# Kernel optimization log

Measured on AMD Instinct MI355X. Metric: run time of the kernel, lower is better.

## Reference

```python
import jax, jax.numpy as jnp
import numpy as np

NU, NS, NG, NW, NT = 100000, 50000, 50, 20000, 10
C, F = 64, 384

def setup_inputs() -> dict:
    key = jax.random.key(0)
    ks = jax.random.split(key, 24)
    s = 0.02
    inp = {
        'reviews': jax.random.normal(ks[0], (NU, F), jnp.float32),
        'overview': jax.random.normal(ks[1], (NS, F), jnp.float32),
        'g_emb': jax.random.normal(ks[2], (NG, C), jnp.float32) * s,
        'w_emb': jax.random.normal(ks[3], (NW, C), jnp.float32) * s,
        't_emb': jax.random.normal(ks[4], (NT, C), jnp.float32) * s,
        'Wu': jax.random.normal(ks[5], (C, F), jnp.float32) * s,
        'bu': jnp.zeros((C,), jnp.float32),
        'Ws': jax.random.normal(ks[6], (C, F), jnp.float32) * s,
        'bs': jnp.zeros((C,), jnp.float32),
        'Wl1': jax.random.normal(ks[7], (8, C, C), jnp.float32) * s,
        'bl1': jnp.zeros((8, C), jnp.float32),
        'Wr1': jax.random.normal(ks[8], (8, C, C), jnp.float32) * s,
        'Wl2': jax.random.normal(ks[9], (8, C, C), jnp.float32) * s,
        'bl2': jnp.zeros((8, C), jnp.float32),
        'Wr2': jax.random.normal(ks[10], (8, C, C), jnp.float32) * s,
        'e_u2s': jnp.stack([jax.random.randint(ks[11], (1000000,), 0, NU, jnp.int32),
                             jax.random.randint(ks[12], (1000000,), 0, NS, jnp.int32)]),
        'e_g2s': jnp.stack([jax.random.randint(ks[13], (150000,), 0, NG, jnp.int32),
                             jax.random.randint(ks[14], (150000,), 0, NS, jnp.int32)]),
        'e_w2s': jnp.stack([jax.random.randint(ks[15], (50000,), 0, NW, jnp.int32),
                             jax.random.randint(ks[16], (50000,), 0, NS, jnp.int32)]),
        'e_t2s': jnp.stack([jax.random.randint(ks[17], (50000,), 0, NT, jnp.int32),
                             jax.random.randint(ks[18], (50000,), 0, NS, jnp.int32)]),
        'eli': jnp.stack([jax.random.randint(ks[19], (200000,), 0, NU, jnp.int32),
                           jax.random.randint(ks[20], (200000,), 0, NS, jnp.int32)]),
    }
    return inp


def _sage_conv(x_src, x_dst, src, dst, Wl, bl, Wr):
    # PyG SAGEConv: lin_l(mean_{neighbors} x_src) + lin_r(x_dst); lin_r has no bias
    n_dst = x_dst.shape[0]
    msg = x_src[src]                                   # [E, C] gather
    agg = jax.ops.segment_sum(msg, dst, num_segments=n_dst)
    cnt = jax.ops.segment_sum(jnp.ones((src.shape[0], 1), x_src.dtype), dst, num_segments=n_dst)
    mean = agg / jnp.maximum(cnt, 1.0)
    return mean @ Wl.T + bl + x_dst @ Wr.T


def _hetero_layer(x, ets, Wl, bl, Wr):
    # to_hetero: per-edge-type SAGEConv, sum-aggregate over edge types per dst node type
    out = {k: None for k in x}
    for i, (st, dt, src, dst) in enumerate(ets):
        o = _sage_conv(x[st], x[dt], src, dst, Wl[i], bl[i], Wr[i])
        out[dt] = o if out[dt] is None else out[dt] + o
    return out


def _forward(reviews, overview, g_emb, w_emb, t_emb, Wu, bu, Ws, bs,
             Wl1, bl1, Wr1, Wl2, bl2, Wr2, e_u2s, e_g2s, e_w2s, e_t2s, eli):
    x = {
        'users': reviews @ Wu.T + bu,
        'series': overview @ Ws.T + bs,
        'genres': g_emb,
        'writer': w_emb,
        'type': t_emb,
    }
    # edge types (fixed order matching the weight stacking): fwd + reverse (ToUndirected)
    ets = [
        ('users', 'series', e_u2s[0], e_u2s[1]),
        ('series', 'users', e_u2s[1], e_u2s[0]),
        ('genres', 'series', e_g2s[0], e_g2s[1]),
        ('series', 'genres', e_g2s[1], e_g2s[0]),
        ('writer', 'series', e_w2s[0], e_w2s[1]),
        ('series', 'writer', e_w2s[1], e_w2s[0]),
        ('type', 'series', e_t2s[0], e_t2s[1]),
        ('series', 'type', e_t2s[1], e_t2s[0]),
    ]
    x = _hetero_layer(x, ets, Wl1, bl1, Wr1)
    x = {k: jax.nn.relu(v) for k, v in x.items()}
    x = _hetero_layer(x, ets, Wl2, bl2, Wr2)
    # Classifier: dot-product scoring on edge_label_index
    src = x['users'][eli[0]]
    dst = x['series'][eli[1]]
    return (src * dst).sum(axis=-1)


def reference(reviews, overview, g_emb, w_emb, t_emb, Wu, bu, Ws, bs,
              Wl1, bl1, Wr1, Wl2, bl2, Wr2, e_u2s, e_g2s, e_w2s, e_t2s, eli):
    return _forward(reviews, overview, g_emb, w_emb, t_emb, Wu, bu, Ws, bs,
                    Wl1, bl1, Wr1, Wl2, bl2, Wr2, e_u2s, e_g2s, e_w2s, e_t2s, eli)
```

## Files before the change

kernel.cpp:

```cpp
#include <hip/hip_runtime.h>

#define NU 100000
#define NS 50000
#define NG 50
#define NW 20000
#define NT 10
#define CDIM 64
#define FDIM 384

typedef short bf16x8 __attribute__((ext_vector_type(8)));
typedef float f32x4 __attribute__((ext_vector_type(4)));
typedef unsigned short ushort;
typedef unsigned int uint;

#define CHUNK 128
#define CSHIFT 7
#define CMASK 127
#define NBINS 2503
#define PSTRIDE 800
#define BTOT 352
#define CTOT 2503
#define W_TOTAL 188416
#define WPB 736

struct PrepArgs {
  const int* src[6];
  const int* dst[6];
  int E[6];
  int nchunk[6];
  int nb[6];
  int cbase[7];
  int bbase[7];
  int cstart[7];
  int* partial;
  int* chunktot;
  int* choff;
  int* bucket[6];
  int* adj[6];
  int* off[6];
};

struct WArgs {
  const float* Wu; const float* Wsp;
  const float* Wl1; const float* Wr1;
  const float* Wl2; const float* Wr2;
  ushort* S;
};

__device__ __forceinline__ void hist_body(const PrepArgs& a, int b, int t, int* bins) {
  int ty = 0;
  while (b >= a.bbase[ty + 1]) ++ty;
  int bl = b - a.bbase[ty], B = a.bbase[ty + 1] - a.bbase[ty];
  int n = a.nchunk[ty], E = a.E[ty];
  const int* __restrict__ dst = a.dst[ty];
  for (int i = t; i < n; i += 256) bins[i] = 0;
  __syncthreads();
  for (int i = bl * 256 + t; i < E; i += B * 256) atomicAdd(&bins[dst[i] >> CSHIFT], 1);
  __syncthreads();
  int* row = a.partial + (size_t)b * PSTRIDE;
  for (int i = t; i < n; i += 256) row[i] = bins[i];
}

__device__ __forceinline__ void scanb_body(const PrepArgs& a, int bin) {
  if (bin >= NBINS) return;
  int ty = 0;
  while (bin >= a.cbase[ty + 1]) ++ty;
  int l = bin - a.cbase[ty];
  int run = 0;
  for (int b = a.bbase[ty]; b < a.bbase[ty + 1]; ++b) {
    int* p = a.partial + (size_t)b * PSTRIDE + l;
    int v = *p;
    *p = run;
    run += v;
  }
  a.chunktot[bin] = run;
}

__device__ __forceinline__ void scanc_body(const PrepArgs& a, int ty, int t, int* sc) {
  int n = a.nchunk[ty];
  int chunk = (n + 255) / 256;
  int lo = t * chunk, hi = min(n, lo + chunk);
  const int* __restrict__ cnt = a.chunktot + a.cbase[ty];
  int s = 0;
  for (int i = lo; i < hi; ++i) s += cnt[i];
  sc[t] = s;
  __syncthreads();
  for (int d = 1; d < 256; d <<= 1) {
    int u = (t >= d) ? sc[t - d] : 0;
    __syncthreads();
    sc[t] += u;
    __syncthreads();
  }
  int* choff = a.choff + a.cbase[ty] + ty;
  int carry = (t > 0) ? sc[t - 1] : 0;
  for (int i = lo; i < hi; ++i) { choff[i] = carry; carry += cnt[i]; }
  if (t == 255) choff[n] = sc[255];
}

__device__ __forceinline__ void fill_body(const PrepArgs& a, int b, int t, int* bins, int* base) {
  int ty = 0;
  while (b >= a.bbase[ty + 1]) ++ty;
  int bl = b - a.bbase[ty], B = a.bbase[ty + 1] - a.bbase[ty];
  int n = a.nchunk[ty], E = a.E[ty];
  const int* __restrict__ dst = a.dst[ty];
  const int* __restrict__ src = a.src[ty];
  int* __restrict__ bucket = a.bucket[ty];
  const int* choff = a.choff + a.cbase[ty] + ty;
  const int* prow = a.partial + (size_t)b * PSTRIDE;
  for (int i = t; i < n; i += 256) { bins[i] = 0; base[i] = choff[i] + prow[i]; }
  __syncthreads();
  for (int i = bl * 256 + t; i < E; i += B * 256) {
    int d = dst[i];
    int l = d >> CSHIFT;
    int r = atomicAdd(&bins[l], 1);
    bucket[base[l] + r] = (src[i] << CSHIFT) | (d & CMASK);
  }
}

__device__ __forceinline__ void csr_body(const PrepArgs& a, int b, int t,
                                         int* bins, int* sc, int* basea) {
  int ty = 0;
  while (b >= a.cstart[ty + 1]) ++ty;
  int c = b - a.cstart[ty];
  const int* __restrict__ bucket = a.bucket[ty];
  const int* choff = a.choff + a.cbase[ty] + ty;
  int beg = choff[c], end = choff[c + 1];
  if (t < CHUNK) bins[t] = 0;
  __syncthreads();
  for (int i = beg + t; i < end; i += 256) atomicAdd(&bins[bucket[i] & CMASK], 1);
  __syncthreads();
  int v = (t < CHUNK) ? bins[t] : 0;
  if (t < CHUNK) sc[t] = v;
  __syncthreads();
#pragma unroll
  for (int d = 1; d < CHUNK; d <<= 1) {
    int u = (t < CHUNK && t >= d) ? sc[t - d] : 0;
    __syncthreads();
    if (t < CHUNK) sc[t] += u;
    __syncthreads();
  }
  if (t < CHUNK) { basea[t] = beg + sc[t] - v; bins[t] = basea[t]; }
  __syncthreads();
  int gbase = c * CHUNK;
  int nb = a.nb[ty];
  if (t < CHUNK && gbase + t < nb) a.off[ty][gbase + t] = basea[t];
  if (b == a.cstart[ty + 1] - 1 && t == 0) a.off[ty][nb] = choff[a.nchunk[ty]];
  int* __restrict__ adj = a.adj[ty];
  for (int i = beg + t; i < end; i += 256) {
    int pk = bucket[i];
    int r = atomicAdd(&bins[pk & CMASK], 1);
    adj[r] = pk >> CSHIFT;
  }
}

__device__ __forceinline__ int swz_src(int u, int F) {
  int p = u >> 11;
  int nt = (u >> 9) & 3;
  int lane = (u >> 3) & 63;
  int j = u & 7;
  int row = nt * 16 + (lane & 15);
  int col = p * 32 + ((lane >> 4) << 3) + j;
  return row * F + col;
}

__device__ __forceinline__ void wprep_body(const WArgs& w, int i) {
  if (i >= W_TOTAL) return;
  float v;
  size_t hbase, lbase;
  int u;
  if (i < 24576) {
    u = i; hbase = 0; lbase = 24576;
    v = w.Wu[swz_src(u, FDIM)];
  } else if (i < 49152) {
    u = i - 24576; hbase = 49152; lbase = 73728;
    v = w.Wsp[swz_src(u, FDIM)];
  } else {
    int j = i - 49152;
    int layer = j / 69632;
    j %= 69632;
    const float* Wl = layer ? w.Wl2 : w.Wl1;
    const float* Wr = layer ? w.Wr2 : w.Wr1;
    size_t base = 98304 + (size_t)layer * 139264;
    if (j < 32768) {
      int s = j >> 12; u = j & 4095;
      hbase = base + (size_t)s * 4096; lbase = base + 32768 + (size_t)s * 4096;
      v = Wl[s * 4096 + swz_src(u, 64)];
    } else if (j < 65536) {
      int q = j - 32768; int s = q >> 12; u = q & 4095;
      hbase = base + 65536 + (size_t)s * 4096; lbase = base + 98304 + (size_t)s * 4096;
      v = Wr[s * 4096 + swz_src(u, 64)];
    } else {
      u = j - 65536;
      hbase = base + 131072; lbase = base + 135168;
      int si = swz_src(u, 64);
      v = Wr[si] + Wr[8192 + si] + Wr[16384 + si] + Wr[24576 + si];
    }
  }
  uint b = __float_as_uint(v);
  uint h = b & 0xFFFF0000u;
  float r = v - __uint_as_float(h);
  w.S[hbase + u] = (ushort)(h >> 16);
  w.S[lbase + u] = (ushort)(__float_as_uint(r) >> 16);
}

__device__ __forceinline__ void csr_gather_body(const int* __restrict__ adj,
                                                const int* __restrict__ off,
                                                const float* __restrict__ x,
                                                float* __restrict__ out,
                                                int wid, int lane) {
  int beg = off[wid], deg = off[wid + 1] - beg;
  float a0 = 0.f, a1 = 0.f, a2 = 0.f, a3 = 0.f;
  int j = 0;
  for (; j + 4 <= deg; j += 4) {
    int s0 = adj[beg + j], s1 = adj[beg + j + 1];
    int s2 = adj[beg + j + 2], s3 = adj[beg + j + 3];
    a0 += x[(size_t)s0 * CDIM + lane];
    a1 += x[(size_t)s1 * CDIM + lane];
    a2 += x[(size_t)s2 * CDIM + lane];
    a3 += x[(size_t)s3 * CDIM + lane];
  }
  for (; j < deg; ++j) a0 += x[(size_t)adj[beg + j] * CDIM + lane];
  float s = (a0 + a1) + (a2 + a3);
  out[(size_t)wid * CDIM + lane] = (deg > 0) ? s / (float)deg : 0.f;
}

struct AggArgs {
  const int* adj[6];
  const int* off[6];
  const float* x[6];
  float* out[6];
  int N[6];
  int start[7];
  int ntask;
};

__global__ __launch_bounds__(256) void agg_fused(AggArgs a) {
  int b = blockIdx.x;
  int ti = 0;
  while (b >= a.start[ti + 1]) ++ti;
  int wid = (b - a.start[ti]) * 4 + (threadIdx.x >> 6);
  int lane = threadIdx.x & 63;
  if (wid >= a.N[ti]) return;
  csr_gather_body(a.adj[ti], a.off[ti], a.x[ti], a.out[ti], wid, lane);
}

struct SmallT { const int* src; const int* dst; int E; const float* x;
                float* partial; int* pcnt; int nd; int G; };
struct Small2T { const float* partial; const int* pcnt; float* out; int nd; int G; };

__device__ __forceinline__ void small1_body(const SmallT& s, int blk, int t, int* smem) {
  float* acc = (float*)smem;
  int* cnt = smem + s.nd * CDIM;
  int lane = t & 63, wv = t >> 6;
  for (int i = t; i < s.nd * CDIM; i += 256) acc[i] = 0.f;
  for (int i = t; i < s.nd; i += 256) cnt[i] = 0;
  __syncthreads();
  const int* __restrict__ src = s.src;
  const int* __restrict__ dst = s.dst;
  const float* __restrict__ x = s.x;
  int E = s.E;
  for (int j0 = (blk * 4 + wv) * 64; j0 < E; j0 += s.G * 256) {
    int myj = j0 + lane;
    int sv = 0, dv = 0;
    if (myj < E) { sv = src[myj]; dv = dst[myj]; }
    int m = min(64, E - j0);
    int j = 0;
    for (; j + 4 <= m; j += 4) {
      int s0 = __shfl(sv, j, 64), s1 = __shfl(sv, j + 1, 64);
      int s2 = __shfl(sv, j + 2, 64), s3 = __shfl(sv, j + 3, 64);
      int d0 = __shfl(dv, j, 64), d1 = __shfl(dv, j + 1, 64);
      int d2 = __shfl(dv, j + 2, 64), d3 = __shfl(dv, j + 3, 64);
      float v0 = x[(size_t)s0 * CDIM + lane];
      float v1 = x[(size_t)s1 * CDIM + lane];
      float v2 = x[(size_t)s2 * CDIM + lane];
      float v3 = x[(size_t)s3 * CDIM + lane];
      atomicAdd(&acc[d0 * CDIM + lane], v0);
      atomicAdd(&acc[d1 * CDIM + lane], v1);
      atomicAdd(&acc[d2 * CDIM + lane], v2);
      atomicAdd(&acc[d3 * CDIM + lane], v3);
      if (lane == 0) {
        atomicAdd(&cnt[d0], 1); atomicAdd(&cnt[d1], 1);
        atomicAdd(&cnt[d2], 1); atomicAdd(&cnt[d3], 1);
      }
    }
    for (; j < m; ++j) {
      int sj = __shfl(sv, j, 64), dj = __shfl(dv, j, 64);
      atomicAdd(&acc[dj * CDIM + lane], x[(size_t)sj * CDIM + lane]);
      if (lane == 0) atomicAdd(&cnt[dj], 1);
    }
  }
  __syncthreads();
  float* po = s.partial + (size_t)blk * s.nd * CDIM;
  for (int i = t; i < s.nd * CDIM; i += 256) po[i] = acc[i];
  int* pc = s.pcnt + blk * s.nd;
  for (int i = t; i < s.nd; i += 256) pc[i] = cnt[i];
}

__device__ __forceinline__ void small2_body(const Small2T& s, int d, int t, int* smem) {
  float* red = (float*)smem;
  int* redc = smem + 256;
  int c = t & 63, sl = t >> 6;
  float sum = 0.f;
  int k = 0;
  for (int g = sl; g < s.G; g += 4) {
    sum += s.partial[(size_t)g * s.nd * CDIM + d * CDIM + c];
    if (c == 0) k += s.pcnt[g * s.nd + d];
  }
  red[sl * 64 + c] = sum;
  if (c == 0) redc[sl] = k;
  __syncthreads();
  if (sl == 0) {
    float tot = red[c] + red[64 + c] + red[128 + c] + red[192 + c];
    int kt = redc[0] + redc[1] + redc[2] + redc[3];
    s.out[d * CDIM + c] = (kt > 0) ? tot / (float)kt : 0.f;
  }
}

struct GSeg { const float* A; const ushort* Wh; const ushort* Wl; int F; };
struct GArgs {
  GSeg seg[5];
  const float* bias[4];
  float* out;
  int nseg, nbias, M, relu;
};
struct GemmMulti { GArgs g[5]; int start[6]; int n; };

__device__ __forceinline__ void split8(const float* __restrict__ p, bf16x8& hi, bf16x8& lo) {
  float4 v0 = *(const float4*)p;
  float4 v1 = *(const float4*)(p + 4);
  float a[8] = {v0.x, v0.y, v0.z, v0.w, v1.x, v1.y, v1.z, v1.w};
  union { uint u[4]; bf16x8 v; } H, L;
#pragma unroll
  for (int i = 0; i < 4; ++i) {
    uint u0 = __float_as_uint(a[2 * i]), u1 = __float_as_uint(a[2 * i + 1]);
    uint h0 = u0 & 0xFFFF0000u, h1 = u1 & 0xFFFF0000u;
    float r0 = a[2 * i] - __uint_as_float(h0);
    float r1 = a[2 * i + 1] - __uint_as_float(h1);
    H.u[i] = (h0 >> 16) | h1;
    L.u[i] = ((__float_as_uint(r0) & 0xFFFF0000u) >> 16) | (__float_as_uint(r1) & 0xFFFF0000u);
  }
  hi = H.v;
  lo = L.v;
}

__device__ __forceinline__ void mfma_body(const GArgs& g, int mb, int tid) {
  const int lane = tid & 63, wv = tid >> 6;
  const int ln = lane & 15, quad = lane >> 4;
  const int m0 = mb * 64;
  f32x4 acc[4];
#pragma unroll
  for (int nt = 0; nt < 4; ++nt) acc[nt] = (f32x4){0.f, 0.f, 0.f, 0.f};

  const int ar = min(m0 + 16 * wv + ln, g.M - 1);

  for (int s = 0; s < g.nseg; ++s) {
    const float* __restrict__ A = g.seg[s].A;
    const ushort* __restrict__ whl = g.seg[s].Wh + (size_t)lane * 8;
    const ushort* __restrict__ wll = g.seg[s].Wl + (size_t)lane * 8;
    const int F = g.seg[s].F;
    const float* ap = A + (size_t)ar * F + quad * 8;
    for (int k0 = 0; k0 < F; k0 += 32) {
      bf16x8 ah, al;
      split8(ap + k0, ah, al);
      const size_t pb = (size_t)(k0 >> 5) * 2048;
#pragma unroll
      for (int nt = 0; nt < 4; ++nt) {
        bf16x8 bh = *(const bf16x8*)(whl + pb + nt * 512);
        bf16x8 bl = *(const bf16x8*)(wll + pb + nt * 512);
        acc[nt] = __builtin_amdgcn_mfma_f32_16x16x32_bf16(ah, bh, acc[nt], 0, 0, 0);
        acc[nt] = __builtin_amdgcn_mfma_f32_16x16x32_bf16(al, bh, acc[nt], 0, 0, 0);
        acc[nt] = __builtin_amdgcn_mfma_f32_16x16x32_bf16(ah, bl, acc[nt], 0, 0, 0);
      }
    }
  }

#pragma unroll
  for (int nt = 0; nt < 4; ++nt) {
    int c = nt * 16 + ln;
    float b = 0.f;
    for (int i = 0; i < g.nbias; ++i) b += g.bias[i][c];
#pragma unroll
    for (int r = 0; r < 4; ++r) {
      int m = m0 + 16 * wv + quad * 4 + r;
      if (m < g.M) {
        float o = acc[nt][r] + b;
        if (g.relu) o = fmaxf(o, 0.f);
        g.out[(size_t)m * CDIM + c] = o;
      }
    }
  }
}

__global__ __launch_bounds__(256) void gemm_multi_k(GemmMulti gm) {
  int b = blockIdx.x;
  int i = 0;
  while (b >= gm.start[i + 1]) ++i;
  mfma_body(gm.g[i], b - gm.start[i], threadIdx.x);
}

__global__ __launch_bounds__(256) void s1_k(PrepArgs pa, WArgs wa) {
  __shared__ int smem[PSTRIDE];
  int b = blockIdx.x;
  if (b < BTOT) hist_body(pa, b, threadIdx.x, smem);
  else wprep_body(wa, (b - BTOT) * 256 + threadIdx.x);
}

__global__ __launch_bounds__(256) void s2_k(PrepArgs pa, GArgs g) {
  int b = blockIdx.x;
  if (b < 10) scanb_body(pa, b * 256 + threadIdx.x);
  else mfma_body(g, b - 10, threadIdx.x);
}

__global__ __launch_bounds__(256) void s3_k(PrepArgs pa, GArgs g) {
  __shared__ int smem[256];
  int b = blockIdx.x;
  if (b < 6) scanc_body(pa, b, threadIdx.x, smem);
  else mfma_body(g, b - 6, threadIdx.x);
}

__global__ __launch_bounds__(256) void s4_k(PrepArgs pa, SmallT sg, SmallT st) {
  __shared__ int smem[3264];
  int b = blockIdx.x;
  if (b < BTOT) fill_body(pa, b, threadIdx.x, smem, smem + PSTRIDE);
  else if (b < BTOT + 256) small1_body(sg, b - BTOT, threadIdx.x, smem);
  else small1_body(st, b - BTOT - 256, threadIdx.x, smem);
}

__global__ __launch_bounds__(256) void s5_k(PrepArgs pa, Small2T g2, Small2T t2) {
  __shared__ int smem[384];
  int b = blockIdx.x;
  if (b < CTOT) csr_body(pa, b, threadIdx.x, smem, smem + CHUNK, smem + 2 * CHUNK);
  else if (b < CTOT + NG) small2_body(g2, b - CTOT, threadIdx.x, smem);
  else small2_body(t2, b - CTOT - NG, threadIdx.x, smem);
}

__global__ __launch_bounds__(256) void score_k(const int* __restrict__ eli, int E,
                                               const float* __restrict__ xu,
                                               const float* __restrict__ xs,
                                               float* __restrict__ out) {
  long long gid = (long long)blockIdx.x * 256 + threadIdx.x;
  int e = (int)(gid >> 6);
  int c = (int)(gid & 63);
  if (e < E) {
    int u = eli[e];
    int sv = eli[E + e];
    float p = xu[(size_t)u * CDIM + c] * xs[(size_t)sv * CDIM + c];
#pragma unroll
    for (int off = 32; off > 0; off >>= 1) p += __shfl_down(p, off, 64);
    if (c == 0) out[e] = p;
  }
}

extern "C" void kernel_launch(void* const* d_in, const int* in_sizes, int n_in,
                              void* d_out, int out_size, void* d_ws, size_t ws_size,
                              hipStream_t stream) {
  const float* reviews  = (const float*)d_in[0];
  const float* overview = (const float*)d_in[1];
  const float* g_emb    = (const float*)d_in[2];
  const float* w_emb    = (const float*)d_in[3];
  const float* t_emb    = (const float*)d_in[4];
  const float* Wu  = (const float*)d_in[5];
  const float* bu  = (const float*)d_in[6];
  const float* Wsp = (const float*)d_in[7];
  const float* bs  = (const float*)d_in[8];
  const float* Wl1 = (const float*)d_in[9];
  const float* bl1 = (const float*)d_in[10];
  const float* Wr1 = (const float*)d_in[11];
  const float* Wl2 = (const float*)d_in[12];
  const float* bl2 = (const float*)d_in[13];
  const float* Wr2 = (const float*)d_in[14];
  const int* e_u2s = (const int*)d_in[15];
  const int* e_g2s = (const int*)d_in[16];
  const int* e_w2s = (const int*)d_in[17];
  const int* e_t2s = (const int*)d_in[18];
  const int* eli   = (const int*)d_in[19];
  const int E_u = in_sizes[15] / 2;
  const int E_g = in_sizes[16] / 2;
  const int E_w = in_sizes[17] / 2;
  const int E_t = in_sizes[18] / 2;
  const int E_l = in_sizes[19] / 2;

  float* ws = (float*)d_ws;
  size_t off = 0;
  auto take = [&](size_t n) { float* p = ws + off; off += n; return p; };
  float* x0u = take((size_t)NU * CDIM);
  float* x0s = take((size_t)NS * CDIM);
  float* x1u = take((size_t)NU * CDIM);
  float* x1s = take((size_t)NS * CDIM);
  float* x1g = take((size_t)NG * CDIM);
  float* x1w = take((size_t)NW * CDIM);
  float* x1t = take((size_t)NT * CDIM);
  float* aggS0 = take((size_t)NS * CDIM);
  float* aggS2 = take((size_t)NS * CDIM);
  float* aggS4 = take((size_t)NS * CDIM);
  float* aggS6 = take((size_t)NS * CDIM);
  float* agg1  = take((size_t)NU * CDIM);
  float* agg5  = take((size_t)NW * CDIM);
  float* agg3  = take((size_t)NG * CDIM);
  float* agg7  = take((size_t)NT * CDIM);
  float* spartG = take((size_t)256 * NG * CDIM);
  int* spcntG   = (int*)take((size_t)256 * NG);
  float* spartT = take((size_t)128 * NT * CDIM);
  int* spcntT   = (int*)take((size_t)128 * NT);
  ushort* wsplit = (ushort*)take((size_t)W_TOTAL);
  int* bkt0 = (int*)take(E_u);
  int* bkt1 = (int*)take(E_u);
  int* bkt2 = (int*)take(E_g);
  int* bkt3 = (int*)take(E_w);
  int* bkt4 = (int*)take(E_w);
  int* bkt5 = (int*)take(E_t);
  int* adj0 = (int*)take(E_u);
  int* adj1 = (int*)take(E_u);
  int* adj2 = (int*)take(E_g);
  int* adj3 = (int*)take(E_w);
  int* adj4 = (int*)take(E_w);
  int* adj5 = (int*)take(E_t);
  int* off0 = (int*)take(NS + 1);
  int* off1 = (int*)take(NU + 1);
  int* off2 = (int*)take(NS + 1);
  int* off3 = (int*)take(NS + 1);
  int* off4 = (int*)take(NW + 1);
  int* off5 = (int*)take(NS + 1);
  int* partial  = (int*)take((size_t)BTOT * PSTRIDE);
  int* chunktot = (int*)take(NBINS);
  int* choffG   = (int*)take(NBINS + 6);
  float* x2u = x0u;
  float* x2s = x0s;

  const ushort* WuH = wsplit + 0;
  const ushort* WuL = wsplit + 24576;
  const ushort* WsH = wsplit + 49152;
  const ushort* WsL = wsplit + 73728;
  auto WlH = [&](int layer, int seg) { return wsplit + 98304 + (size_t)layer * 139264 + (size_t)seg * 4096; };
  auto WlL = [&](int layer, int seg) { return wsplit + 98304 + (size_t)layer * 139264 + 32768 + (size_t)seg * 4096; };
  auto WrH = [&](int layer, int seg) { return wsplit + 98304 + (size_t)layer * 139264 + 65536 + (size_t)seg * 4096; };
  auto WrL = [&](int layer, int seg) { return wsplit + 98304 + (size_t)layer * 139264 + 98304 + (size_t)seg * 4096; };
  auto WrsH = [&](int layer) { return wsplit + 98304 + (size_t)layer * 139264 + 131072; };
  auto WrsL = [&](int layer) { return wsplit + 98304 + (size_t)layer * 139264 + 135168; };

  PrepArgs pa{};
  const int* bsrc[6] = {e_u2s, e_u2s + E_u, e_g2s, e_w2s, e_w2s + E_w, e_t2s};
  const int* bdst[6] = {e_u2s + E_u, e_u2s, e_g2s + E_g, e_w2s + E_w, e_w2s, e_t2s + E_t};
  int bE[6]  = {E_u, E_u, E_g, E_w, E_w, E_t};
  int nch[6] = {391, 782, 391, 391, 157, 391};
  int cb[7]  = {0, 391, 1173, 1564, 1955, 2112, 2503};
  int bpt[6] = {128, 128, 32, 16, 16, 32};
  int nbT[6] = {NS, NU, NS, NS, NW, NS};
  int* bkts[6] = {bkt0, bkt1, bkt2, bkt3, bkt4, bkt5};
  int* adjs[6] = {adj0, adj1, adj2, adj3, adj4, adj5};
  int* offs[6] = {off0, off1, off2, off3, off4, off5};
  int bb = 0, cs = 0;
  for (int i = 0; i < 6; ++i) {
    pa.src[i] = bsrc[i]; pa.dst[i] = bdst[i]; pa.E[i] = bE[i];
    pa.nchunk[i] = nch[i]; pa.nb[i] = nbT[i]; pa.cbase[i] = cb[i];
    pa.bbase[i] = bb; bb += bpt[i];
    pa.cstart[i] = cs; cs += nch[i];
    pa.bucket[i] = bkts[i]; pa.adj[i] = adjs[i]; pa.off[i] = offs[i];
  }
  pa.cbase[6] = cb[6]; pa.bbase[6] = bb; pa.cstart[6] = cs;
  pa.partial = partial; pa.chunktot = chunktot; pa.choff = choffG;

  WArgs wa{Wu, Wsp, Wl1, Wr1, Wl2, Wr2, wsplit};

  s1_k<<<BTOT + WPB, 256, 0, stream>>>(pa, wa);

  {
    GArgs g{};
    g.seg[0] = {reviews, WuH, WuL, FDIM}; g.nseg = 1;
    g.bias[0] = bu; g.nbias = 1;
    g.out = x0u; g.M = NU; g.relu = 0;
    s2_k<<<10 + (NU + 63) / 64, 256, 0, stream>>>(pa, g);
  }
  {
    GArgs g{};
    g.seg[0] = {overview, WsH, WsL, FDIM}; g.nseg = 1;
    g.bias[0] = bs; g.nbias = 1;
    g.out = x0s; g.M = NS; g.relu = 0;
    s3_k<<<6 + (NS + 63) / 64, 256, 0, stream>>>(pa, g);
  }
  {
    SmallT sg{e_g2s, e_g2s + E_g, E_g, x0s, spartG, spcntG, NG, 256};
    SmallT st{e_t2s, e_t2s + E_t, E_t, x0s, spartT, spcntT, NT, 128};
    sg.src = e_g2s + E_g; sg.dst = e_g2s;
    st.src = e_t2s + E_t; st.dst = e_t2s;
    s4_k<<<BTOT + 256 + 128, 256, 0, stream>>>(pa, sg, st);
  }
  {
    Small2T g2{spartG, spcntG, agg3, NG, 256};
    Small2T t2{spartT, spcntT, agg7, NT, 128};
    s5_k<<<CTOT + NG + NT, 256, 0, stream>>>(pa, g2, t2);
  }
  {
    AggArgs a{};
    const int* aadj[6] = {adj0, adj1, adj4, adj2, adj3, adj5};
    const int* aoff[6] = {off0, off1, off4, off2, off3, off5};
    const float* ax[6] = {x0u, x0s, x0s, g_emb, w_emb, t_emb};
    float* aout[6] = {aggS0, agg1, agg5, aggS2, aggS4, aggS6};
    int aN[6] = {NS, NU, NW, NS, NS, NS};
    int s = 0;
    for (int i = 0; i < 6; ++i) {
      a.adj[i] = aadj[i]; a.off[i] = aoff[i]; a.x[i] = ax[i];
      a.out[i] = aout[i]; a.N[i] = aN[i];
      a.start[i] = s; s += (aN[i] + 3) / 4;
    }
    a.start[6] = s; a.ntask = 6;
    agg_fused<<<s, 256, 0, stream>>>(a);
  }
  {
    GemmMulti gm{};
    gm.g[0].seg[0] = {aggS0, WlH(0, 0), WlL(0, 0), 64};
    gm.g[0].seg[1] = {aggS2, WlH(0, 2), WlL(0, 2), 64};
    gm.g[0].seg[2] = {aggS4, WlH(0, 4), WlL(0, 4), 64};
    gm.g[0].seg[3] = {aggS6, WlH(0, 6), WlL(0, 6), 64};
    gm.g[0].seg[4] = {x0s, WrsH(0), WrsL(0), 64};
    gm.g[0].nseg = 5;
    gm.g[0].bias[0] = bl1 + 0 * 64; gm.g[0].bias[1] = bl1 + 2 * 64;
    gm.g[0].bias[2] = bl1 + 4 * 64; gm.g[0].bias[3] = bl1 + 6 * 64; gm.g[0].nbias = 4;
    gm.g[0].out = x1s; gm.g[0].M = NS; gm.g[0].relu = 1;
    gm.g[1].seg[0] = {agg1, WlH(0, 1), WlL(0, 1), 64};
    gm.g[1].seg[1] = {x0u, WrH(0, 1), WrL(0, 1), 64};
    gm.g[1].nseg = 2;
    gm.g[1].bias[0] = bl1 + 1 * 64; gm.g[1].nbias = 1;
    gm.g[1].out = x1u; gm.g[1].M = NU; gm.g[1].relu = 1;
    gm.g[2].seg[0] = {agg5, WlH(0, 5), WlL(0, 5), 64};
    gm.g[2].seg[1] = {w_emb, WrH(0, 5), WrL(0, 5), 64};
    gm.g[2].nseg = 2;
    gm.g[2].bias[0] = bl1 + 5 * 64; gm.g[2].nbias = 1;
    gm.g[2].out = x1w; gm.g[2].M = NW; gm.g[2].relu = 1;
    gm.g[3].seg[0] = {agg3, WlH(0, 3), WlL(0, 3), 64};
    gm.g[3].seg[1] = {g_emb, WrH(0, 3), WrL(0, 3), 64};
    gm.g[3].nseg = 2;
    gm.g[3].bias[0] = bl1 + 3 * 64; gm.g[3].nbias = 1;
    gm.g[3].out = x1g; gm.g[3].M = NG; gm.g[3].relu = 1;
    gm.g[4].seg[0] = {agg7, WlH(0, 7), WlL(0, 7), 64};
    gm.g[4].seg[1] = {t_emb, WrH(0, 7), WrL(0, 7), 64};
    gm.g[4].nseg = 2;
    gm.g[4].bias[0] = bl1 + 7 * 64; gm.g[4].nbias = 1;
    gm.g[4].out = x1t; gm.g[4].M = NT; gm.g[4].relu = 1;
    int mb[5] = {(NS + 63) / 64, (NU + 63) / 64, (NW + 63) / 64, 1, 1};
    int s = 0;
    for (int i = 0; i < 5; ++i) { gm.start[i] = s; s += mb[i]; }
    gm.start[5] = s; gm.n = 5;
    gemm_multi_k<<<s, 256, 0, stream>>>(gm);
  }
  {
    AggArgs a{};
    const int* aadj[5] = {adj0, adj2, adj3, adj5, adj1};
    const int* aoff[5] = {off0, off2, off3, off5, off1};
    const float* ax[5] = {x1u, x1g, x1w, x1t, x1s};
    float* aout[5] = {aggS0, aggS2, aggS4, aggS6, agg1};
    int aN[5] = {NS, NS, NS, NS, NU};
    int s = 0;
    for (int i = 0; i < 5; ++i) {
      a.adj[i] = aadj[i]; a.off[i] = aoff[i]; a.x[i] = ax[i];
      a.out[i] = aout[i]; a.N[i] = aN[i];
      a.start[i] = s; s += (aN[i] + 3) / 4;
    }
    a.start[5] = s; a.start[6] = s; a.ntask = 5;
    agg_fused<<<s, 256, 0, stream>>>(a);
  }
  {
    GemmMulti gm{};
    gm.g[0].seg[0] = {aggS0, WlH(1, 0), WlL(1, 0), 64};
    gm.g[0].seg[1] = {aggS2, WlH(1, 2), WlL(1, 2), 64};
    gm.g[0].seg[2] = {aggS4, WlH(1, 4), WlL(1, 4), 64};
    gm.g[0].seg[3] = {aggS6, WlH(1, 6), WlL(1, 6), 64};
    gm.g[0].seg[4] = {x1s, WrsH(1), WrsL(1), 64};
    gm.g[0].nseg = 5;
    gm.g[0].bias[0] = bl2 + 0 * 64; gm.g[0].bias[1] = bl2 + 2 * 64;
    gm.g[0].bias[2] = bl2 + 4 * 64; gm.g[0].bias[3] = bl2 + 6 * 64; gm.g[0].nbias = 4;
    gm.g[0].out = x2s; gm.g[0].M = NS; gm.g[0].relu = 0;
    gm.g[1].seg[0] = {agg1, WlH(1, 1), WlL(1, 1), 64};
    gm.g[1].seg[1] = {x1u, WrH(1, 1), WrL(1, 1), 64};
    gm.g[1].nseg = 2;
    gm.g[1].bias[0] = bl2 + 1 * 64; gm.g[1].nbias = 1;
    gm.g[1].out = x2u; gm.g[1].M = NU; gm.g[1].relu = 0;
    int s = 0;
    gm.start[0] = 0; s += (NS + 63) / 64;
    gm.start[1] = s; s += (NU + 63) / 64;
    gm.start[2] = s; gm.start[3] = s; gm.start[4] = s; gm.start[5] = s;
    gm.n = 2;
    gemm_multi_k<<<s, 256, 0, stream>>>(gm);
  }
  score_k<<<((long long)E_l * 64 + 255) / 256, 256, 0, stream>>>(
      eli, E_l, x2u, x2s, (float*)d_out);
}
```

Before: 892.3 us.

## Aggregate directly from chunk buckets with LDS atomics, dropping CSR adjacency scatter

Removes the per-chunk scatter that built the adj arrays in csr_body. Aggregation now works from the dst-chunk buckets: each 512-thread block owns a 128-node chunk and accumulates neighbour rows into a padded LDS tile with float atomics, using float4 loads. It then scales each row by the inverse degree taken from off. This saves the adj write/read traffic and a pass in prep, at the cost of many LDS atomics and possible load imbalance between chunks.

```diff
diff --git a/kernel.cpp b/kernel.cpp
--- a/kernel.cpp
+++ b/kernel.cpp
@@ -22,6 +22,7 @@
 #define CTOT 2503
 #define W_TOTAL 188416
 #define WPB 736
+#define ACCS 65
 
 struct PrepArgs {
   const int* src[6];
@@ -36,7 +37,6 @@
   int* chunktot;
   int* choff;
   int* bucket[6];
-  int* adj[6];
   int* off[6];
 };
 
@@ -118,7 +118,7 @@
 }
 
 __device__ __forceinline__ void csr_body(const PrepArgs& a, int b, int t,
-                                         int* bins, int* sc, int* basea) {
+                                         int* bins, int* sc) {
   int ty = 0;
   while (b >= a.cstart[ty + 1]) ++ty;
   int c = b - a.cstart[ty];
@@ -139,18 +139,10 @@
     if (t < CHUNK) sc[t] += u;
     __syncthreads();
   }
-  if (t < CHUNK) { basea[t] = beg + sc[t] - v; bins[t] = basea[t]; }
-  __syncthreads();
   int gbase = c * CHUNK;
   int nb = a.nb[ty];
-  if (t < CHUNK && gbase + t < nb) a.off[ty][gbase + t] = basea[t];
+  if (t < CHUNK && gbase + t < nb) a.off[ty][gbase + t] = beg + sc[t] - v;
   if (b == a.cstart[ty + 1] - 1 && t == 0) a.off[ty][nb] = choff[a.nchunk[ty]];
-  int* __restrict__ adj = a.adj[ty];
-  for (int i = beg + t; i < end; i += 256) {
-    int pk = bucket[i];
-    int r = atomicAdd(&bins[pk & CMASK], 1);
-    adj[r] = pk >> CSHIFT;
-  }
 }
 
 __device__ __forceinline__ int swz_src(int u, int F) {
@@ -203,45 +195,87 @@
   w.S[lbase + u] = (ushort)(__float_as_uint(r) >> 16);
 }
 
-__device__ __forceinline__ void csr_gather_body(const int* __restrict__ adj,
-                                                const int* __restrict__ off,
-                                                const float* __restrict__ x,
-                                                float* __restrict__ out,
-                                                int wid, int lane) {
-  int beg = off[wid], deg = off[wid + 1] - beg;
-  float a0 = 0.f, a1 = 0.f, a2 = 0.f, a3 = 0.f;
-  int j = 0;
-  for (; j + 4 <= deg; j += 4) {
-    int s0 = adj[beg + j], s1 = adj[beg + j + 1];
-    int s2 = adj[beg + j + 2], s3 = adj[beg + j + 3];
-    a0 += x[(size_t)s0 * CDIM + lane];
-    a1 += x[(size_t)s1 * CDIM + lane];
-    a2 += x[(size_t)s2 * CDIM + lane];
-    a3 += x[(size_t)s3 * CDIM + lane];
-  }
-  for (; j < deg; ++j) a0 += x[(size_t)adj[beg + j] * CDIM + lane];
-  float s = (a0 + a1) + (a2 + a3);
-  out[(size_t)wid * CDIM + lane] = (deg > 0) ? s / (float)deg : 0.f;
-}
-
-struct AggArgs {
-  const int* adj[6];
-  const int* off[6];
+struct AggCArgs {
+  const int* bucket[6];
+  const int* choff[6];
+  const int* offp[6];
   const float* x[6];
   float* out[6];
   int N[6];
   int start[7];
-  int ntask;
 };
 
-__global__ __launch_bounds__(256) void agg_fused(AggArgs a) {
+__global__ __launch_bounds__(512) void aggc_k(AggCArgs a) {
+  __shared__ float acc[CHUNK * ACCS];
+  __shared__ float inv[CHUNK];
   int b = blockIdx.x;
   int ti = 0;
   while (b >= a.start[ti + 1]) ++ti;
-  int wid = (b - a.start[ti]) * 4 + (threadIdx.x >> 6);
-  int lane = threadIdx.x & 63;
-  if (wid >= a.N[ti]) return;
-  csr_gather_body(a.adj[ti], a.off[ti], a.x[ti], a.out[ti], wid, lane);
+  int c = b - a.start[ti];
+  const int* __restrict__ bucket = a.bucket[ti];
+  const int* choff = a.choff[ti];
+  int beg = choff[c], end = choff[c + 1];
+  int t = threadIdx.x;
+  int gbase = c * CHUNK;
+  int N = a.N[ti];
+  for (int i = t; i < CHUNK * ACCS; i += 512) acc[i] = 0.f;
+  if (t < CHUNK) {
+    int r = gbase + t;
+    float iv = 0.f;
+    if (r < N) {
+      int d = a.offp[ti][r + 1] - a.offp[ti][r];
+      iv = (d > 0) ? 1.f / (float)d : 0.f;
+    }
+    inv[t] = iv;
+  }
+  __syncthreads();
+  const float* __restrict__ x = a.x[ti];
+  int lane = t & 63, wv = t >> 6;
+  int g = lane >> 4, l4 = lane & 15;
+  for (int i0 = beg + wv * 64; i0 < end; i0 += 8 * 64) {
+    int i = i0 + lane;
+    int pk = (i < end) ? bucket[i] : -1;
+    int m = min(64, end - i0);
+    int j = 0;
+    for (; j + 16 <= m; j += 16) {
+      int pg0 = __shfl(pk, j + 0 + g, 64);
+      int pg1 = __shfl(pk, j + 4 + g, 64);
+      int pg2 = __shfl(pk, j + 8 + g, 64);
+      int pg3 = __shfl(pk, j + 12 + g, 64);
+      float4 v0 = *(const float4*)(x + (((size_t)(pg0 >> CSHIFT)) << 6) + l4 * 4);
+      float4 v1 = *(const float4*)(x + (((size_t)(pg1 >> CSHIFT)) << 6) + l4 * 4);
+      float4 v2 = *(const float4*)(x + (((size_t)(pg2 >> CSHIFT)) << 6) + l4 * 4);
+      float4 v3 = *(const float4*)(x + (((size_t)(pg3 >> CSHIFT)) << 6) + l4 * 4);
+      float* q0 = &acc[(pg0 & CMASK) * ACCS + l4 * 4];
+      float* q1 = &acc[(pg1 & CMASK) * ACCS + l4 * 4];
+      float* q2 = &acc[(pg2 & CMASK) * ACCS + l4 * 4];
+      float* q3 = &acc[(pg3 & CMASK) * ACCS + l4 * 4];
+      atomicAdd(q0 + 0, v0.x); atomicAdd(q0 + 1, v0.y);
+      atomicAdd(q0 + 2, v0.z); atomicAdd(q0 + 3, v0.w);
+      atomicAdd(q1 + 0, v1.x); atomicAdd(q1 + 1, v1.y);
+      atomicAdd(q1 + 2, v1.z); atomicAdd(q1 + 3, v1.w);
+      atomicAdd(q2 + 0, v2.x); atomicAdd(q2 + 1, v2.y);
+      atomicAdd(q2 + 2, v2.z); atomicAdd(q2 + 3, v2.w);
+      atomicAdd(q3 + 0, v3.x); atomicAdd(q3 + 1, v3.y);
+      atomicAdd(q3 + 2, v3.z); atomicAdd(q3 + 3, v3.w);
+    }
+    for (; j < m; j += 4) {
+      int idx = j + g;
+      int pg = __shfl(pk, idx & 63, 64);
+      if (idx < m) {
+        float4 v = *(const float4*)(x + (((size_t)(pg >> CSHIFT)) << 6) + l4 * 4);
+        float* q = &acc[(pg & CMASK) * ACCS + l4 * 4];
+        atomicAdd(q + 0, v.x); atomicAdd(q + 1, v.y);
+        atomicAdd(q + 2, v.z); atomicAdd(q + 3, v.w);
+      }
+    }
+  }
+  __syncthreads();
+  float* __restrict__ out = a.out[ti];
+  for (int idx = t; idx < CHUNK * CDIM; idx += 512) {
+    int r = idx >> 6, ch = idx & 63;
+    if (gbase + r < N) out[(((size_t)(gbase + r)) << 6) + ch] = acc[r * ACCS + ch] * inv[r];
+  }
 }
 
 struct SmallT { const int* src; const int* dst; int E; const float* x;
@@ -429,7 +463,7 @@
 __global__ __launch_bounds__(256) void s5_k(PrepArgs pa, Small2T g2, Small2T t2) {
   __shared__ int smem[384];
   int b = blockIdx.x;
-  if (b < CTOT) csr_body(pa, b, threadIdx.x, smem, smem + CHUNK, smem + 2 * CHUNK);
+  if (b < CTOT) csr_body(pa, b, threadIdx.x, smem, smem + CHUNK);
   else if (b < CTOT + NG) small2_body(g2, b - CTOT, threadIdx.x, smem);
   else small2_body(t2, b - CTOT - NG, threadIdx.x, smem);
 }
@@ -509,12 +543,6 @@
   int* bkt3 = (int*)take(E_w);
   int* bkt4 = (int*)take(E_w);
   int* bkt5 = (int*)take(E_t);
-  int* adj0 = (int*)take(E_u);
-  int* adj1 = (int*)take(E_u);
-  int* adj2 = (int*)take(E_g);
-  int* adj3 = (int*)take(E_w);
-  int* adj4 = (int*)take(E_w);
-  int* adj5 = (int*)take(E_t);
   int* off0 = (int*)take(NS + 1);
   int* off1 = (int*)take(NU + 1);
   int* off2 = (int*)take(NS + 1);
@@ -547,7 +575,6 @@
   int bpt[6] = {128, 128, 32, 16, 16, 32};
   int nbT[6] = {NS, NU, NS, NS, NW, NS};
   int* bkts[6] = {bkt0, bkt1, bkt2, bkt3, bkt4, bkt5};
-  int* adjs[6] = {adj0, adj1, adj2, adj3, adj4, adj5};
   int* offs[6] = {off0, off1, off2, off3, off4, off5};
   int bb = 0, cs = 0;
   for (int i = 0; i < 6; ++i) {
@@ -555,7 +582,7 @@
     pa.nchunk[i] = nch[i]; pa.nb[i] = nbT[i]; pa.cbase[i] = cb[i];
     pa.bbase[i] = bb; bb += bpt[i];
     pa.cstart[i] = cs; cs += nch[i];
-    pa.bucket[i] = bkts[i]; pa.adj[i] = adjs[i]; pa.off[i] = offs[i];
+    pa.bucket[i] = bkts[i]; pa.off[i] = offs[i];
   }
   pa.cbase[6] = cb[6]; pa.bbase[6] = bb; pa.cstart[6] = cs;
   pa.partial = partial; pa.chunktot = chunktot; pa.choff = choffG;
@@ -591,20 +618,23 @@
     s5_k<<<CTOT + NG + NT, 256, 0, stream>>>(pa, g2, t2);
   }
   {
-    AggArgs a{};
-    const int* aadj[6] = {adj0, adj1, adj4, adj2, adj3, adj5};
-    const int* aoff[6] = {off0, off1, off4, off2, off3, off5};
-    const float* ax[6] = {x0u, x0s, x0s, g_emb, w_emb, t_emb};
-    float* aout[6] = {aggS0, agg1, agg5, aggS2, aggS4, aggS6};
-    int aN[6] = {NS, NU, NW, NS, NS, NS};
+    AggCArgs a{};
+    int tys[6] = {0, 1, 2, 3, 4, 5};
+    const float* ax[6] = {x0u, x0s, g_emb, w_emb, x0s, t_emb};
+    float* aout[6] = {aggS0, agg1, aggS2, aggS4, agg5, aggS6};
     int s = 0;
     for (int i = 0; i < 6; ++i) {
-      a.adj[i] = aadj[i]; a.off[i] = aoff[i]; a.x[i] = ax[i];
-      a.out[i] = aout[i]; a.N[i] = aN[i];
-      a.start[i] = s; s += (aN[i] + 3) / 4;
-    }
-    a.start[6] = s; a.ntask = 6;
-    agg_fused<<<s, 256, 0, stream>>>(a);
+      int ty = tys[i];
+      a.bucket[i] = bkts[ty];
+      a.choff[i] = choffG + cb[ty] + ty;
+      a.offp[i] = offs[ty];
+      a.x[i] = ax[i];
+      a.out[i] = aout[i];
+      a.N[i] = nbT[ty];
+      a.start[i] = s; s += nch[ty];
+    }
+    a.start[6] = s;
+    aggc_k<<<s, 512, 0, stream>>>(a);
   }
   {
     GemmMulti gm{};
@@ -644,20 +674,23 @@
     gemm_multi_k<<<s, 256, 0, stream>>>(gm);
   }
   {
-    AggArgs a{};
-    const int* aadj[5] = {adj0, adj2, adj3, adj5, adj1};
-    const int* aoff[5] = {off0, off2, off3, off5, off1};
+    AggCArgs a{};
+    int tys[5] = {0, 2, 3, 5, 1};
     const float* ax[5] = {x1u, x1g, x1w, x1t, x1s};
     float* aout[5] = {aggS0, aggS2, aggS4, aggS6, agg1};
-    int aN[5] = {NS, NS, NS, NS, NU};
     int s = 0;
     for (int i = 0; i < 5; ++i) {
-      a.adj[i] = aadj[i]; a.off[i] = aoff[i]; a.x[i] = ax[i];
-      a.out[i] = aout[i]; a.N[i] = aN[i];
-      a.start[i] = s; s += (aN[i] + 3) / 4;
-    }
-    a.start[5] = s; a.start[6] = s; a.ntask = 5;
-    agg_fused<<<s, 256, 0, stream>>>(a);
+      int ty = tys[i];
+      a.bucket[i] = bkts[ty];
+      a.choff[i] = choffG + cb[ty] + ty;
+      a.offp[i] = offs[ty];
+      a.x[i] = ax[i];
+      a.out[i] = aout[i];
+      a.N[i] = nbT[ty];
+      a.start[i] = s; s += nch[ty];
+    }
+    a.start[5] = s; a.start[6] = s;
+    aggc_k<<<s, 512, 0, stream>>>(a);
   }
   {
     GemmMulti gm{};
```

Result: slower. 2.311 ms (+159.0%).
